# Performance work log

Measured on AMD Instinct MI355X. Metric: run time of the kernel, lower is better.

The kernel has to match this reference:

```python
import jax, jax.numpy as jnp
import numpy as np

ALPHA = 4.0  # spikingjelly surrogate.Sigmoid default
TAU = 2.0    # LIFNode default

@jax.custom_vjp
def spike(x):
    return (x >= 0).astype(x.dtype)

def _spike_fwd(x):
    return spike(x), x

def _spike_bwd(x, g):
    s = jax.nn.sigmoid(ALPHA * x)
    return (g * ALPHA * s * (1.0 - s),)

spike.defvjp(_spike_fwd, _spike_bwd)

def lif(x_seq, v_th):
    # multi-step LIF over leading time dim; decay_input=True, v_reset=0 (hard reset)
    def step(v, x):
        v = v + (x - v) / TAU
        s = spike(v - v_th)
        return v * (1.0 - s), s
    _, s_seq = jax.lax.scan(step, jnp.zeros_like(x_seq[0]), x_seq)
    return s_seq

def bn_c(x, gamma, beta, mean, var, eps=1e-5):
    # eval-mode BatchNorm1d over channel axis 2 of [T,N,C,V]
    inv = (gamma / jnp.sqrt(var + eps))[None, None, :, None]
    return (x - mean[None, None, :, None]) * inv + beta[None, None, :, None]

def conv1x1(x, w):
    # 1x1 Conv1d == channel mixing: w [Cout,Cin], x [T,N,C,V]
    return jnp.einsum('oc,tncv->tnov', w, x)

def setup_inputs() -> dict:
    key = jax.random.key(0)
    T, N, C, V = 4, 512, 256, 25
    ks = jax.random.split(key, 24)
    def bn_params(k1, k2, k3, k4):
        return (jax.random.uniform(k1, (C,)) * 0.5 + 0.75,
                jax.random.normal(k2, (C,)) * 0.1,
                jax.random.normal(k3, (C,)) * 0.1,
                jax.random.uniform(k4, (C,)) * 0.5 + 0.5)
    x = jax.random.normal(ks[0], (T, N, C, V), dtype=jnp.float32)
    s = 1.0 / np.sqrt(C)
    wq = jax.random.normal(ks[1], (C, C)) * s
    wk = jax.random.normal(ks[2], (C, C)) * s
    wv = jax.random.normal(ks[3], (C, C)) * s
    wp = jax.random.normal(ks[4], (C, C)) * s
    bp = jax.random.normal(ks[5], (C,)) * 0.02
    qg, qb, qm, qvar = bn_params(ks[6], ks[7], ks[8], ks[9])
    kg, kb, km, kvar = bn_params(ks[10], ks[11], ks[12], ks[13])
    vg, vb, vm, vvar = bn_params(ks[14], ks[15], ks[16], ks[17])
    pg, pb, pm, pvar = bn_params(ks[18], ks[19], ks[20], ks[21])
    return dict(x=x, wq=wq, wk=wk, wv=wv, wp=wp, bp=bp,
                qg=qg, qb=qb, qm=qm, qvar=qvar,
                kg=kg, kb=kb, km=km, kvar=kvar,
                vg=vg, vb=vb, vm=vm, vvar=vvar,
                pg=pg, pb=pb, pm=pm, pvar=pvar)

def reference(x, wq, wk, wv, wp, bp, qg, qb, qm, qvar, kg, kb, km, kvar,
              vg, vb, vm, vvar, pg, pb, pm, pvar):
    T, N, C, V = x.shape
    H = 8
    D = C // H
    scale = 0.125

    def branch(w, g, b, m, var):
        s = lif(bn_c(conv1x1(x, w), g, b, m, var), 1.0)       # [T,N,C,V]
        # -> [T,N,V,C] -> [T,N,V,H,D] -> [T,N,H,V,D]
        return jnp.transpose(s, (0, 1, 3, 2)).reshape(T, N, V, H, D).transpose(0, 1, 3, 2, 4)

    q = branch(wq, qg, qb, qm, qvar)
    k = branch(wk, kg, kb, km, kvar)
    v = branch(wv, vg, vb, vm, vvar)

    attn = jnp.einsum('tnhvd,tnhwd->tnhvw', q, k)            # binary spike attn, no softmax
    y = jnp.einsum('tnhvw,tnhwd->tnhvd', attn, v) * scale    # [T,N,H,V,D]
    y = y.transpose(0, 1, 2, 4, 3).reshape(T, N, C, V)       # transpose(3,4) then merge H*D=C
    y = lif(y, 0.5)                                          # attn_lif, v_threshold=0.5
    y = conv1x1(y, wp) + bp[None, None, :, None]             # proj_conv (bias=True)
    y = lif(bn_c(y, pg, pb, pm, pvar), 1.0)                  # proj_bn + proj_lif
    return y + x                                             # residual
```

## Files before the change

### kernel.cpp

```cpp
#include <hip/hip_runtime.h>
#include <cstdint>
#include <cstddef>

#define T_ 4
#define N_ 512
#define C_ 256
#define V_ 25
#define H_ 8

typedef _Float16 half8_t __attribute__((ext_vector_type(8)));
typedef float f32x16 __attribute__((ext_vector_type(16)));

__device__ __forceinline__ f32x16 mfma16(half8_t a, half8_t b, f32x16 c) {
  return __builtin_amdgcn_mfma_f32_32x32x16_f16(a, b, c, 0, 0, 0);
}

__global__ void kw_stage(const float* __restrict__ wq, const float* __restrict__ wk,
                         const float* __restrict__ wv, const float* __restrict__ wp,
                         const float* __restrict__ qg, const float* __restrict__ qvar,
                         const float* __restrict__ kg, const float* __restrict__ kvar,
                         const float* __restrict__ vg, const float* __restrict__ vvar,
                         const float* __restrict__ pg, const float* __restrict__ pvar,
                         _Float16* __restrict__ Wstg) {
  int i = blockIdx.x * 512 + threadIdx.x;
  int j = i & 7, lane = (i >> 3) & 63, rt = (i >> 9) & 3, m = (i >> 11) & 1;
  int s = (i >> 12) & 3, p = (i >> 14) & 3, c = i >> 16;
  int kt = p * 4 + s;
  int row = rt * 32 + (lane & 31);
  int k = kt * 16 + (lane >> 5) * 8 + j;
  const float *w, *g, *va;
  int grow;
  if (c < 6) {
    int br = c >> 1;
    w = br == 0 ? wq : br == 1 ? wk : wv;
    g = br == 0 ? qg : br == 1 ? kg : vg;
    va = br == 0 ? qvar : br == 1 ? kvar : vvar;
    grow = (c & 1) * 128 + row;
  } else {
    w = wp; g = pg; va = pvar;
    grow = (c - 6) * 128 + row;
  }
  float sc = g[grow] / sqrtf(va[grow] + 1e-5f);
  float wv_ = w[grow * 256 + k] * sc;
  _Float16 hi = (_Float16)wv_;
  Wstg[i] = (m == 0) ? hi : (_Float16)(wv_ - (float)hi);
}

#define STAGE_A(gidx, bufsel)                                                     \
  do {                                                                            \
    const _Float16* sp_ = Wstg + (size_t)(gidx) * 16384 + tid * 8;                \
    char* dp_ = Abuf + (bufsel) * 32768 + tid * 16;                               \
    __builtin_amdgcn_global_load_lds((const uint32_t*)(sp_),          (uint32_t*)(dp_),          16, 0, 0); \
    __builtin_amdgcn_global_load_lds((const uint32_t*)(sp_ + 4096),   (uint32_t*)(dp_ + 8192),   16, 0, 0); \
    __builtin_amdgcn_global_load_lds((const uint32_t*)(sp_ + 8192),   (uint32_t*)(dp_ + 16384),  16, 0, 0); \
    __builtin_amdgcn_global_load_lds((const uint32_t*)(sp_ + 12288),  (uint32_t*)(dp_ + 24576),  16, 0, 0); \
  } while (0)

__launch_bounds__(512, 1)
__global__ void k1_mfma(const float* __restrict__ x, const _Float16* __restrict__ Wstg,
                        const float* __restrict__ qg, const float* __restrict__ qb,
                        const float* __restrict__ qm, const float* __restrict__ qvar,
                        const float* __restrict__ kg, const float* __restrict__ kb,
                        const float* __restrict__ km, const float* __restrict__ kvar,
                        const float* __restrict__ vg, const float* __restrict__ vb,
                        const float* __restrict__ vm, const float* __restrict__ vvar,
                        uint32_t* __restrict__ masks) {
  __shared__ __align__(16) char LDSb[102400 + 25856 + 512];
  float* Xf = (float*)LDSb;
  char* Abuf = LDSb;
  float* Ms = (float*)(LDSb + 102400);
  float* bic = (float*)(LDSb + 102400 + 25856);

  const int n = blockIdx.x, tid = threadIdx.x;
  const int lane = tid & 63, wid = tid >> 6;
  const int rg = wid >> 2, cg = wid & 3;
  const int lr = lane & 31, lkg = lane >> 5;

  for (int t = 0; t < 4; ++t) {
    const float* sp = x + (size_t)(t * N_ + n) * 6400;
    float* dp = Xf + t * 6400;
    for (int i = tid; i < 1600; i += 512)
      __builtin_amdgcn_global_load_lds((const uint32_t*)(sp + i * 4), (uint32_t*)(dp + i * 4), 16, 0, 0);
  }
  __syncthreads();

  half8_t Bf0[16], Bf1[16];
  {
    int col = cg * 32 + lr;
    bool valid = col < 100;
    int tq = valid ? col / 25 : 0;
    int v = valid ? col - tq * 25 : 0;
    const float* xb = Xf + tq * 6400 + v;
#pragma unroll
    for (int kt = 0; kt < 16; ++kt) {
#pragma unroll
      for (int jj = 0; jj < 8; ++jj) {
        int k = kt * 16 + lkg * 8 + jj;
        float f = xb[k * 25];
        f = valid ? f : 0.0f;
        _Float16 hi = (_Float16)f;
        Bf0[kt][jj] = hi;
        Bf1[kt][jj] = (_Float16)(f - (float)hi);
      }
    }
  }
  __syncthreads();
  STAGE_A(0, 0);

  for (int c = 0; c < 6; ++c) {
    if (tid < 128) {
      int ch = (c & 1) * 128 + tid;
      const int br = c >> 1;
      const float* g  = br == 0 ? qg : br == 1 ? kg : vg;
      const float* be = br == 0 ? qb : br == 1 ? kb : vb;
      const float* mu = br == 0 ? qm : br == 1 ? km : vm;
      const float* va = br == 0 ? qvar : br == 1 ? kvar : vvar;
      float sc = g[ch] / sqrtf(va[ch] + 1e-5f);
      bic[tid] = be[ch] - mu[ch] * sc;
    }
    f32x16 acc0 = {}, acc1 = {};
#pragma unroll
    for (int p = 0; p < 4; ++p) {
      __syncthreads();
      int gnext = c * 4 + p + 1;
      if (gnext < 24) STAGE_A(gnext, (p + 1) & 1);
#pragma unroll
      for (int s = 0; s < 4; ++s) {
        const char* kb = Abuf + (p & 1) * 32768 + s * 8192;
        half8_t A00 = *(const half8_t*)(kb + 0    + 2 * rg * 1024 + lane * 16);
        half8_t A01 = *(const half8_t*)(kb + 0    + (2 * rg + 1) * 1024 + lane * 16);
        half8_t A10 = *(const half8_t*)(kb + 4096 + 2 * rg * 1024 + lane * 16);
        half8_t A11 = *(const half8_t*)(kb + 4096 + (2 * rg + 1) * 1024 + lane * 16);
        int kt = p * 4 + s;
        __builtin_amdgcn_s_setprio(1);
        acc0 = mfma16(A00, Bf0[kt], acc0);
        acc1 = mfma16(A01, Bf0[kt], acc1);
        acc0 = mfma16(A00, Bf1[kt], acc0);
        acc1 = mfma16(A01, Bf1[kt], acc1);
        acc0 = mfma16(A10, Bf0[kt], acc0);
        acc1 = mfma16(A11, Bf0[kt], acc1);
        __builtin_amdgcn_s_setprio(0);
      }
    }

    const int br = c >> 1;
    for (int ph = 0; ph < 2; ++ph) {
      __syncthreads();
      if (rg == ph) {
        int col = cg * 32 + lr;
        if (col < 100) {
#pragma unroll
          for (int rr = 0; rr < 16; ++rr) {
            int rowc = (rr & 3) + 8 * (rr >> 2) + 4 * lkg;
            Ms[rowc * 101 + col] = acc0[rr] + bic[ph * 64 + rowc];
            Ms[(32 + rowc) * 101 + col] = acc1[rr] + bic[ph * 64 + 32 + rowc];
          }
        }
      }
      __syncthreads();
      const int d = lane & 31, sub = lane >> 5;
      for (int it = 0; it < 4; ++it) {
        int ti = it * 16 + wid * 2 + sub;
        bool valid = ti < 50;
        int hl = valid ? ti / 25 : 0;
        int v = valid ? ti - hl * 25 : 0;
        int row = hl * 32 + d;
        float st = 0.0f;
#pragma unroll
        for (int t = 0; t < 4; ++t) {
          float cu = Ms[row * 101 + t * 25 + v];
          st += (cu - st) * 0.5f;
          bool sbit = valid && (st >= 1.0f);
          if (st >= 1.0f) st = 0.0f;
          unsigned long long b = __ballot(sbit);
          if (valid && (lane == 0 || lane == 32)) {
            uint32_t wd = (lane == 0) ? (uint32_t)b : (uint32_t)(b >> 32);
            int hg = (c & 1) * 4 + ph * 2 + hl;
            masks[((((size_t)t * N_ + n) * 3 + br) * H_ + hg) * V_ + v] = wd;
          }
        }
      }
    }
  }
}

__launch_bounds__(64)
__global__ void k2_attn(const uint32_t* __restrict__ masks, uint32_t* __restrict__ mask2) {
  __shared__ uint32_t qs[T_][V_], ks_[T_][V_], vs[T_][V_];
  const int n = blockIdx.x >> 3;
  const int h = blockIdx.x & 7;
  const int l = threadIdx.x;
  for (int i = l; i < T_ * 3 * V_; i += 64) {
    int t = i / (3 * V_);
    int r = i - t * (3 * V_);
    int br = r / V_;
    int v = r - br * V_;
    uint32_t w = masks[(((size_t)t * N_ + n) * 3 + br) * (H_ * V_) + h * V_ + v];
    if (br == 0) qs[t][v] = w;
    else if (br == 1) ks_[t][v] = w;
    else vs[t][v] = w;
  }
  __syncthreads();
  const int hi = l >> 5, d = l & 31;
  for (int vv = 0; vv < 13; ++vv) {
    int v = vv * 2 + hi;
    bool valid = (v < V_);
    int vc = valid ? v : 0;
    float st = 0.0f;
#pragma unroll
    for (int t = 0; t < 4; ++t) {
      int y = 0;
      uint32_t qmw = qs[t][vc];
#pragma unroll
      for (int w = 0; w < V_; ++w) {
        int a = __popc(qmw & ks_[t][w]);
        y += a * (int)((vs[t][w] >> d) & 1u);
      }
      float yf = 0.125f * (float)y;
      st += (yf - st) * 0.5f;
      bool s = valid && (st >= 0.5f);
      if (st >= 0.5f) st = 0.0f;
      unsigned long long b = __ballot(s);
      if (valid && (l == 0 || l == 32)) {
        uint32_t wd = (l == 0) ? (uint32_t)b : (uint32_t)(b >> 32);
        mask2[(((size_t)t * N_ + n) * V_ + v) * H_ + h] = wd;
      }
    }
  }
}

__launch_bounds__(512, 1)
__global__ void k3_mfma(const float* __restrict__ x, const _Float16* __restrict__ Wstg,
                        const uint32_t* __restrict__ mask2, const float* __restrict__ bp,
                        const float* __restrict__ pg, const float* __restrict__ pb,
                        const float* __restrict__ pm, const float* __restrict__ pvar,
                        float* __restrict__ out) {
  __shared__ __align__(16) char LDSb[65536 + 25856 + 512 + 3200];
  char* Abuf = LDSb;
  float* Ms = (float*)(LDSb + 65536);
  float* bic = (float*)(LDSb + 65536 + 25856);
  uint32_t* m2s = (uint32_t*)(LDSb + 65536 + 25856 + 512);

  const int n = blockIdx.x, tid = threadIdx.x;
  const int lane = tid & 63, wid = tid >> 6;
  const int rg = wid >> 2, cg = wid & 3;
  const int lr = lane & 31, lkg = lane >> 5;

  for (int i = tid; i < 800; i += 512) {
    int t = i / 200, r = i - t * 200;
    m2s[i] = mask2[(size_t)(t * N_ + n) * 200 + r];
  }
  __syncthreads();

  half8_t Bf[16];
  {
    int col = cg * 32 + lr;
    bool valid = col < 100;
    int tq = valid ? col / 25 : 0;
    int v = valid ? col - tq * 25 : 0;
#pragma unroll
    for (int kt = 0; kt < 16; ++kt) {
#pragma unroll
      for (int jj = 0; jj < 8; ++jj) {
        int k = kt * 16 + lkg * 8 + jj;
        uint32_t bit = (m2s[tq * 200 + v * 8 + (k >> 5)] >> (k & 31)) & 1u;
        Bf[kt][jj] = (valid && bit) ? (_Float16)1.0f : (_Float16)0.0f;
      }
    }
  }
  STAGE_A(24, 0);

  for (int c = 0; c < 2; ++c) {
    if (tid < 128) {
      int ch = c * 128 + tid;
      float sc = pg[ch] / sqrtf(pvar[ch] + 1e-5f);
      bic[tid] = fmaf(bp[ch] - pm[ch], sc, pb[ch]);
    }
    f32x16 acc0 = {}, acc1 = {};
#pragma unroll
    for (int p = 0; p < 4; ++p) {
      __syncthreads();
      int gnext = (6 + c) * 4 + p + 1;
      if (gnext < 32) STAGE_A(gnext, (p + 1) & 1);
#pragma unroll
      for (int s = 0; s < 4; ++s) {
        const char* kb = Abuf + (p & 1) * 32768 + s * 8192;
        half8_t A00 = *(const half8_t*)(kb + 0    + 2 * rg * 1024 + lane * 16);
        half8_t A01 = *(const half8_t*)(kb + 0    + (2 * rg + 1) * 1024 + lane * 16);
        half8_t A10 = *(const half8_t*)(kb + 4096 + 2 * rg * 1024 + lane * 16);
        half8_t A11 = *(const half8_t*)(kb + 4096 + (2 * rg + 1) * 1024 + lane * 16);
        int kt = p * 4 + s;
        __builtin_amdgcn_s_setprio(1);
        acc0 = mfma16(A00, Bf[kt], acc0);
        acc1 = mfma16(A01, Bf[kt], acc1);
        acc0 = mfma16(A10, Bf[kt], acc0);
        acc1 = mfma16(A11, Bf[kt], acc1);
        __builtin_amdgcn_s_setprio(0);
      }
    }

    for (int ph = 0; ph < 2; ++ph) {
      __syncthreads();
      if (rg == ph) {
        int col = cg * 32 + lr;
        if (col < 100) {
#pragma unroll
          for (int rr = 0; rr < 16; ++rr) {
            int rowc = (rr & 3) + 8 * (rr >> 2) + 4 * lkg;
            Ms[rowc * 101 + col] = acc0[rr] + bic[ph * 64 + rowc];
            Ms[(32 + rowc) * 101 + col] = acc1[rr] + bic[ph * 64 + 32 + rowc];
          }
        }
      }
      __syncthreads();
      const int d = lane & 31, sub = lane >> 5;
      for (int it = 0; it < 4; ++it) {
        int ti = it * 16 + wid * 2 + sub;
        if (ti < 50) {
          int hl = ti / 25, v = ti - hl * 25;
          int row = hl * 32 + d;
          float st = 0.0f;
#pragma unroll
          for (int t = 0; t < 4; ++t) {
            float cu = Ms[row * 101 + t * 25 + v];
            st += (cu - st) * 0.5f;
            float s = (st >= 1.0f) ? 1.0f : 0.0f;
            if (st >= 1.0f) st = 0.0f;
            Ms[row * 101 + t * 25 + v] = s;
          }
        }
      }
      __syncthreads();
      for (int ii = tid; ii < 6400; ii += 512) {
        int t = ii / 1600, r2 = ii - t * 1600;
        int cl = r2 / 25, v = r2 - cl * 25;
        size_t go = (size_t)(t * N_ + n) * 6400 + (size_t)(c * 128 + ph * 64 + cl) * 25 + v;
        out[go] = Ms[cl * 101 + t * 25 + v] + x[go];
      }
    }
  }
}

extern "C" void kernel_launch(void* const* d_in, const int* in_sizes, int n_in,
                              void* d_out, int out_size, void* d_ws, size_t ws_size,
                              hipStream_t stream) {
  const float* x    = (const float*)d_in[0];
  const float* wq   = (const float*)d_in[1];
  const float* wk   = (const float*)d_in[2];
  const float* wv   = (const float*)d_in[3];
  const float* wp   = (const float*)d_in[4];
  const float* bp   = (const float*)d_in[5];
  const float* qg   = (const float*)d_in[6];
  const float* qb   = (const float*)d_in[7];
  const float* qm   = (const float*)d_in[8];
  const float* qvar = (const float*)d_in[9];
  const float* kg   = (const float*)d_in[10];
  const float* kb   = (const float*)d_in[11];
  const float* km   = (const float*)d_in[12];
  const float* kvar = (const float*)d_in[13];
  const float* vg   = (const float*)d_in[14];
  const float* vb   = (const float*)d_in[15];
  const float* vm   = (const float*)d_in[16];
  const float* vvar = (const float*)d_in[17];
  const float* pg   = (const float*)d_in[18];
  const float* pb   = (const float*)d_in[19];
  const float* pm   = (const float*)d_in[20];
  const float* pvar = (const float*)d_in[21];

  _Float16* Wstg  = (_Float16*)d_ws;
  uint32_t* masks = (uint32_t*)d_ws + 262144;
  uint32_t* mask2 = masks + 1228800;

  kw_stage<<<1024, 512, 0, stream>>>(wq, wk, wv, wp, qg, qvar, kg, kvar,
                                     vg, vvar, pg, pvar, Wstg);
  k1_mfma<<<512, 512, 0, stream>>>(x, Wstg, qg, qb, qm, qvar, kg, kb, km, kvar,
                                   vg, vb, vm, vvar, masks);
  k2_attn<<<4096, 64, 0, stream>>>(masks, mask2);
  k3_mfma<<<512, 512, 0, stream>>>(x, Wstg, mask2, bp, pg, pb, pm, pvar, (float*)d_out);
}
```

Baseline: 275.0 us.

## Pre-split x into fp16 hi/lo staging and retile MFMA waves with swizzled LDS epilogue

Adds a kx_stage kernel that converts x to fp16 hi/lo pairs in a column-major (v,t)-ordered layout, so k1 loads its B fragments directly from global memory instead of staging fp32 x through LDS and splitting it in registers. Both k1 and k3 reassign waves so each wave owns one 32-row tile and two 32-column tiles, halving A-fragment LDS reads per MFMA. The full 128-row result is written to an XOR-swizzled LDS buffer with float4 stores in a single pass instead of two 64-row phases, and the BN bias is added in the LIF pass. The cost is an extra kernel launch and an extra global round trip for x (about 50MB of workspace), plus more B registers per thread.

```diff
diff --git a/kernel.cpp b/kernel.cpp
--- a/kernel.cpp
+++ b/kernel.cpp
@@ -46,6 +46,33 @@
   Wstg[i] = (m == 0) ? hi : (_Float16)(wv_ - (float)hi);
 }
 
+__global__ void kx_stage(const float* __restrict__ x, _Float16* __restrict__ X16) {
+  __shared__ float Xt[256 * 28];
+  const int n = blockIdx.x, tid = threadIdx.x;
+  for (int t = 0; t < 4; ++t) {
+    __syncthreads();
+    for (int i = tid; i < 6400; i += 256) {
+      int k = i / 25, v = i - k * 25;
+      Xt[k * 28 + v] = x[(size_t)(t * N_ + n) * 6400 + i];
+    }
+    __syncthreads();
+    for (int j = tid; j < 800; j += 256) {
+      int v = j >> 5, kb = j & 31, k0 = kb * 8;
+      half8_t hi, lo;
+#pragma unroll
+      for (int e = 0; e < 8; ++e) {
+        float f = Xt[(k0 + e) * 28 + v];
+        _Float16 h = (_Float16)f;
+        hi[e] = h;
+        lo[e] = (_Float16)(f - (float)h);
+      }
+      size_t base = ((size_t)(2 * n) * 100 + (v * 4 + t)) * 256 + k0;
+      *(half8_t*)(X16 + base) = hi;
+      *(half8_t*)(X16 + base + 25600) = lo;
+    }
+  }
+}
+
 #define STAGE_A(gidx, bufsel)                                                     \
   do {                                                                            \
     const _Float16* sp_ = Wstg + (size_t)(gidx) * 16384 + tid * 8;                \
@@ -56,8 +83,10 @@
     __builtin_amdgcn_global_load_lds((const uint32_t*)(sp_ + 12288),  (uint32_t*)(dp_ + 24576),  16, 0, 0); \
   } while (0)
 
+#define MS_BYTE(colx, rowx) ((colx) * 256 + (((rowx) * 4) ^ (((colx) & 7) << 4)))
+
 __launch_bounds__(512, 1)
-__global__ void k1_mfma(const float* __restrict__ x, const _Float16* __restrict__ Wstg,
+__global__ void k1_mfma(const _Float16* __restrict__ X16, const _Float16* __restrict__ Wstg,
                         const float* __restrict__ qg, const float* __restrict__ qb,
                         const float* __restrict__ qm, const float* __restrict__ qvar,
                         const float* __restrict__ kg, const float* __restrict__ kb,
@@ -65,119 +94,99 @@
                         const float* __restrict__ vg, const float* __restrict__ vb,
                         const float* __restrict__ vm, const float* __restrict__ vvar,
                         uint32_t* __restrict__ masks) {
-  __shared__ __align__(16) char LDSb[102400 + 25856 + 512];
-  float* Xf = (float*)LDSb;
+  __shared__ __align__(16) char LDSb[65536 + 32768 + 512];
   char* Abuf = LDSb;
-  float* Ms = (float*)(LDSb + 102400);
-  float* bic = (float*)(LDSb + 102400 + 25856);
+  char* MsB = LDSb + 65536;
+  float* bic = (float*)(LDSb + 65536 + 32768);
 
   const int n = blockIdx.x, tid = threadIdx.x;
   const int lane = tid & 63, wid = tid >> 6;
-  const int rg = wid >> 2, cg = wid & 3;
+  const int rt = wid & 3, cp = wid >> 2;
   const int lr = lane & 31, lkg = lane >> 5;
 
-  for (int t = 0; t < 4; ++t) {
-    const float* sp = x + (size_t)(t * N_ + n) * 6400;
-    float* dp = Xf + t * 6400;
-    for (int i = tid; i < 1600; i += 512)
-      __builtin_amdgcn_global_load_lds((const uint32_t*)(sp + i * 4), (uint32_t*)(dp + i * 4), 16, 0, 0);
-  }
-  __syncthreads();
-
-  half8_t Bf0[16], Bf1[16];
-  {
-    int col = cg * 32 + lr;
-    bool valid = col < 100;
-    int tq = valid ? col / 25 : 0;
-    int v = valid ? col - tq * 25 : 0;
-    const float* xb = Xf + tq * 6400 + v;
+  half8_t Bh[32], Bl[32];
+#pragma unroll
+  for (int ct = 0; ct < 2; ++ct) {
+    int col = cp * 64 + ct * 32 + lr;
+    int colc = col < 100 ? col : 99;
+    const _Float16* bp0 = X16 + ((size_t)(2 * n) * 100 + colc) * 256 + lkg * 8;
 #pragma unroll
     for (int kt = 0; kt < 16; ++kt) {
-#pragma unroll
-      for (int jj = 0; jj < 8; ++jj) {
-        int k = kt * 16 + lkg * 8 + jj;
-        float f = xb[k * 25];
-        f = valid ? f : 0.0f;
-        _Float16 hi = (_Float16)f;
-        Bf0[kt][jj] = hi;
-        Bf1[kt][jj] = (_Float16)(f - (float)hi);
-      }
-    }
-  }
-  __syncthreads();
+      Bh[ct * 16 + kt] = *(const half8_t*)(bp0 + kt * 16);
+      Bl[ct * 16 + kt] = *(const half8_t*)(bp0 + 25600 + kt * 16);
+    }
+  }
   STAGE_A(0, 0);
 
   for (int c = 0; c < 6; ++c) {
-    if (tid < 128) {
-      int ch = (c & 1) * 128 + tid;
-      const int br = c >> 1;
-      const float* g  = br == 0 ? qg : br == 1 ? kg : vg;
-      const float* be = br == 0 ? qb : br == 1 ? kb : vb;
-      const float* mu = br == 0 ? qm : br == 1 ? km : vm;
-      const float* va = br == 0 ? qvar : br == 1 ? kvar : vvar;
-      float sc = g[ch] / sqrtf(va[ch] + 1e-5f);
-      bic[tid] = be[ch] - mu[ch] * sc;
-    }
+    const int br = c >> 1;
     f32x16 acc0 = {}, acc1 = {};
 #pragma unroll
     for (int p = 0; p < 4; ++p) {
       __syncthreads();
+      if (p == 0 && tid < 128) {
+        int ch = (c & 1) * 128 + tid;
+        const float* g  = br == 0 ? qg : br == 1 ? kg : vg;
+        const float* be = br == 0 ? qb : br == 1 ? kb : vb;
+        const float* mu = br == 0 ? qm : br == 1 ? km : vm;
+        const float* va = br == 0 ? qvar : br == 1 ? kvar : vvar;
+        float sc = g[ch] / sqrtf(va[ch] + 1e-5f);
+        bic[tid] = be[ch] - mu[ch] * sc;
+      }
       int gnext = c * 4 + p + 1;
       if (gnext < 24) STAGE_A(gnext, (p + 1) & 1);
 #pragma unroll
       for (int s = 0; s < 4; ++s) {
-        const char* kb = Abuf + (p & 1) * 32768 + s * 8192;
-        half8_t A00 = *(const half8_t*)(kb + 0    + 2 * rg * 1024 + lane * 16);
-        half8_t A01 = *(const half8_t*)(kb + 0    + (2 * rg + 1) * 1024 + lane * 16);
-        half8_t A10 = *(const half8_t*)(kb + 4096 + 2 * rg * 1024 + lane * 16);
-        half8_t A11 = *(const half8_t*)(kb + 4096 + (2 * rg + 1) * 1024 + lane * 16);
-        int kt = p * 4 + s;
+        const char* kb = Abuf + (p & 1) * 32768 + s * 8192 + rt * 1024 + lane * 16;
+        half8_t Ahi = *(const half8_t*)(kb);
+        half8_t Alo = *(const half8_t*)(kb + 4096);
+        const int kt = p * 4 + s;
         __builtin_amdgcn_s_setprio(1);
-        acc0 = mfma16(A00, Bf0[kt], acc0);
-        acc1 = mfma16(A01, Bf0[kt], acc1);
-        acc0 = mfma16(A00, Bf1[kt], acc0);
-        acc1 = mfma16(A01, Bf1[kt], acc1);
-        acc0 = mfma16(A10, Bf0[kt], acc0);
-        acc1 = mfma16(A11, Bf0[kt], acc1);
+        acc0 = mfma16(Ahi, Bh[kt], acc0);
+        acc1 = mfma16(Ahi, Bh[16 + kt], acc1);
+        acc0 = mfma16(Ahi, Bl[kt], acc0);
+        acc1 = mfma16(Ahi, Bl[16 + kt], acc1);
+        acc0 = mfma16(Alo, Bh[kt], acc0);
+        acc1 = mfma16(Alo, Bh[16 + kt], acc1);
         __builtin_amdgcn_s_setprio(0);
       }
     }
 
-    const int br = c >> 1;
-    for (int ph = 0; ph < 2; ++ph) {
-      __syncthreads();
-      if (rg == ph) {
-        int col = cg * 32 + lr;
-        if (col < 100) {
-#pragma unroll
-          for (int rr = 0; rr < 16; ++rr) {
-            int rowc = (rr & 3) + 8 * (rr >> 2) + 4 * lkg;
-            Ms[rowc * 101 + col] = acc0[rr] + bic[ph * 64 + rowc];
-            Ms[(32 + rowc) * 101 + col] = acc1[rr] + bic[ph * 64 + 32 + rowc];
-          }
+    __syncthreads();
+#pragma unroll
+    for (int ct = 0; ct < 2; ++ct) {
+      int col = cp * 64 + ct * 32 + lr;
+      if (col < 100) {
+        f32x16 A = ct ? acc1 : acc0;
+#pragma unroll
+        for (int qq = 0; qq < 4; ++qq) {
+          int rowb = rt * 32 + qq * 8 + lkg * 4;
+          float4 vq = make_float4(A[qq * 4], A[qq * 4 + 1], A[qq * 4 + 2], A[qq * 4 + 3]);
+          *(float4*)(MsB + MS_BYTE(col, rowb)) = vq;
         }
       }
-      __syncthreads();
-      const int d = lane & 31, sub = lane >> 5;
-      for (int it = 0; it < 4; ++it) {
-        int ti = it * 16 + wid * 2 + sub;
-        bool valid = ti < 50;
-        int hl = valid ? ti / 25 : 0;
-        int v = valid ? ti - hl * 25 : 0;
-        int row = hl * 32 + d;
-        float st = 0.0f;
-#pragma unroll
-        for (int t = 0; t < 4; ++t) {
-          float cu = Ms[row * 101 + t * 25 + v];
-          st += (cu - st) * 0.5f;
-          bool sbit = valid && (st >= 1.0f);
-          if (st >= 1.0f) st = 0.0f;
-          unsigned long long b = __ballot(sbit);
-          if (valid && (lane == 0 || lane == 32)) {
-            uint32_t wd = (lane == 0) ? (uint32_t)b : (uint32_t)(b >> 32);
-            int hg = (c & 1) * 4 + ph * 2 + hl;
-            masks[((((size_t)t * N_ + n) * 3 + br) * H_ + hg) * V_ + v] = wd;
-          }
+    }
+    __syncthreads();
+    const int d = lane & 31, hl = lane >> 5;
+    for (int it = 0; it < 7; ++it) {
+      int task = it * 16 + wid * 2 + hl;
+      bool valid = task < 100;
+      int hg = valid ? task / 25 : 0;
+      int v = valid ? task - hg * 25 : 0;
+      int row = hg * 32 + d;
+      float bicv = bic[hg * 32 + d];
+      float st = 0.0f;
+#pragma unroll
+      for (int t = 0; t < 4; ++t) {
+        int colx = v * 4 + t;
+        float cu = *(const float*)(MsB + MS_BYTE(colx, row)) + bicv;
+        st += (cu - st) * 0.5f;
+        bool sb = valid && (st >= 1.0f);
+        if (st >= 1.0f) st = 0.0f;
+        unsigned long long b = __ballot(sb);
+        if (valid && (lane == 0 || lane == 32)) {
+          uint32_t wd = (lane == 0) ? (uint32_t)b : (uint32_t)(b >> 32);
+          masks[((((size_t)t * N_ + n) * 3 + br) * H_ + (c & 1) * 4 + hg) * V_ + v] = wd;
         }
       }
     }
@@ -235,15 +244,15 @@
                         const float* __restrict__ pg, const float* __restrict__ pb,
                         const float* __restrict__ pm, const float* __restrict__ pvar,
                         float* __restrict__ out) {
-  __shared__ __align__(16) char LDSb[65536 + 25856 + 512 + 3200];
+  __shared__ __align__(16) char LDSb[65536 + 32768 + 512 + 3200];
   char* Abuf = LDSb;
-  float* Ms = (float*)(LDSb + 65536);
-  float* bic = (float*)(LDSb + 65536 + 25856);
-  uint32_t* m2s = (uint32_t*)(LDSb + 65536 + 25856 + 512);
+  char* MsB = LDSb + 65536;
+  float* bic = (float*)(LDSb + 65536 + 32768);
+  uint32_t* m2s = (uint32_t*)(LDSb + 65536 + 32768 + 512);
 
   const int n = blockIdx.x, tid = threadIdx.x;
   const int lane = tid & 63, wid = tid >> 6;
-  const int rg = wid >> 2, cg = wid & 3;
+  const int rt = wid & 3, cp = wid >> 2;
   const int lr = lane & 31, lkg = lane >> 5;
 
   for (int i = tid; i < 800; i += 512) {
@@ -252,91 +261,97 @@
   }
   __syncthreads();
 
-  half8_t Bf[16];
-  {
-    int col = cg * 32 + lr;
+  half8_t Bb[32];
+#pragma unroll
+  for (int ct = 0; ct < 2; ++ct) {
+    int col = cp * 64 + ct * 32 + lr;
     bool valid = col < 100;
-    int tq = valid ? col / 25 : 0;
-    int v = valid ? col - tq * 25 : 0;
+    int v = valid ? (col >> 2) : 0;
+    int t = valid ? (col & 3) : 0;
 #pragma unroll
     for (int kt = 0; kt < 16; ++kt) {
 #pragma unroll
       for (int jj = 0; jj < 8; ++jj) {
         int k = kt * 16 + lkg * 8 + jj;
-        uint32_t bit = (m2s[tq * 200 + v * 8 + (k >> 5)] >> (k & 31)) & 1u;
-        Bf[kt][jj] = (valid && bit) ? (_Float16)1.0f : (_Float16)0.0f;
+        uint32_t bit = (m2s[t * 200 + v * 8 + (k >> 5)] >> (k & 31)) & 1u;
+        Bb[ct * 16 + kt][jj] = (valid && bit) ? (_Float16)1.0f : (_Float16)0.0f;
       }
     }
   }
   STAGE_A(24, 0);
 
   for (int c = 0; c < 2; ++c) {
-    if (tid < 128) {
-      int ch = c * 128 + tid;
-      float sc = pg[ch] / sqrtf(pvar[ch] + 1e-5f);
-      bic[tid] = fmaf(bp[ch] - pm[ch], sc, pb[ch]);
-    }
     f32x16 acc0 = {}, acc1 = {};
 #pragma unroll
     for (int p = 0; p < 4; ++p) {
       __syncthreads();
+      if (p == 0 && tid < 128) {
+        int ch = c * 128 + tid;
+        float sc = pg[ch] / sqrtf(pvar[ch] + 1e-5f);
+        bic[tid] = fmaf(bp[ch] - pm[ch], sc, pb[ch]);
+      }
       int gnext = (6 + c) * 4 + p + 1;
       if (gnext < 32) STAGE_A(gnext, (p + 1) & 1);
 #pragma unroll
       for (int s = 0; s < 4; ++s) {
-        const char* kb = Abuf + (p & 1) * 32768 + s * 8192;
-        half8_t A00 = *(const half8_t*)(kb + 0    + 2 * rg * 1024 + lane * 16);
-        half8_t A01 = *(const half8_t*)(kb + 0    + (2 * rg + 1) * 1024 + lane * 16);
-        half8_t A10 = *(const half8_t*)(kb + 4096 + 2 * rg * 1024 + lane * 16);
-        half8_t A11 = *(const half8_t*)(kb + 4096 + (2 * rg + 1) * 1024 + lane * 16);
-        int kt = p * 4 + s;
+        const char* kb = Abuf + (p & 1) * 32768 + s * 8192 + rt * 1024 + lane * 16;
+        half8_t Ahi = *(const half8_t*)(kb);
+        half8_t Alo = *(const half8_t*)(kb + 4096);
+        const int kt = p * 4 + s;
         __builtin_amdgcn_s_setprio(1);
-        acc0 = mfma16(A00, Bf[kt], acc0);
-        acc1 = mfma16(A01, Bf[kt], acc1);
-        acc0 = mfma16(A10, Bf[kt], acc0);
-        acc1 = mfma16(A11, Bf[kt], acc1);
+        acc0 = mfma16(Ahi, Bb[kt], acc0);
+        acc1 = mfma16(Ahi, Bb[16 + kt], acc1);
+        acc0 = mfma16(Alo, Bb[kt], acc0);
+        acc1 = mfma16(Alo, Bb[16 + kt], acc1);
         __builtin_amdgcn_s_setprio(0);
       }
     }
 
-    for (int ph = 0; ph < 2; ++ph) {
-      __syncthreads();
-      if (rg == ph) {
-        int col = cg * 32 + lr;
-        if (col < 100) {
-#pragma unroll
-          for (int rr = 0; rr < 16; ++rr) {
-            int rowc = (rr & 3) + 8 * (rr >> 2) + 4 * lkg;
-            Ms[rowc * 101 + col] = acc0[rr] + bic[ph * 64 + rowc];
-            Ms[(32 + rowc) * 101 + col] = acc1[rr] + bic[ph * 64 + 32 + rowc];
-          }
+    __syncthreads();
+#pragma unroll
+    for (int ct = 0; ct < 2; ++ct) {
+      int col = cp * 64 + ct * 32 + lr;
+      if (col < 100) {
+        f32x16 A = ct ? acc1 : acc0;
+#pragma unroll
+        for (int qq = 0; qq < 4; ++qq) {
+          int rowb = rt * 32 + qq * 8 + lkg * 4;
+          float4 vq = make_float4(A[qq * 4], A[qq * 4 + 1], A[qq * 4 + 2], A[qq * 4 + 3]);
+          *(float4*)(MsB + MS_BYTE(col, rowb)) = vq;
         }
       }
-      __syncthreads();
-      const int d = lane & 31, sub = lane >> 5;
-      for (int it = 0; it < 4; ++it) {
-        int ti = it * 16 + wid * 2 + sub;
-        if (ti < 50) {
-          int hl = ti / 25, v = ti - hl * 25;
-          int row = hl * 32 + d;
-          float st = 0.0f;
-#pragma unroll
-          for (int t = 0; t < 4; ++t) {
-            float cu = Ms[row * 101 + t * 25 + v];
-            st += (cu - st) * 0.5f;
-            float s = (st >= 1.0f) ? 1.0f : 0.0f;
-            if (st >= 1.0f) st = 0.0f;
-            Ms[row * 101 + t * 25 + v] = s;
-          }
+    }
+    __syncthreads();
+    const int d = lane & 31, hl = lane >> 5;
+    for (int it = 0; it < 7; ++it) {
+      int task = it * 16 + wid * 2 + hl;
+      bool valid = task < 100;
+      int hg = valid ? task / 25 : 0;
+      int v = valid ? task - hg * 25 : 0;
+      int row = hg * 32 + d;
+      float bicv = bic[hg * 32 + d];
+      float st = 0.0f;
+#pragma unroll
+      for (int t = 0; t < 4; ++t) {
+        int colx = v * 4 + t;
+        char* mp = MsB + MS_BYTE(colx, row);
+        if (valid) {
+          float cu = *(const float*)(mp) + bicv;
+          st += (cu - st) * 0.5f;
+          float sv = (st >= 1.0f) ? 1.0f : 0.0f;
+          if (st >= 1.0f) st = 0.0f;
+          *(float*)(mp) = sv;
         }
       }
-      __syncthreads();
-      for (int ii = tid; ii < 6400; ii += 512) {
-        int t = ii / 1600, r2 = ii - t * 1600;
-        int cl = r2 / 25, v = r2 - cl * 25;
-        size_t go = (size_t)(t * N_ + n) * 6400 + (size_t)(c * 128 + ph * 64 + cl) * 25 + v;
-        out[go] = Ms[cl * 101 + t * 25 + v] + x[go];
-      }
+    }
+    __syncthreads();
+    for (int ii = tid; ii < 12800; ii += 512) {
+      int t = ii / 3200, r2 = ii - t * 3200;
+      int cl = r2 / 25, v = r2 - cl * 25;
+      int colx = v * 4 + t;
+      float sv = *(const float*)(MsB + MS_BYTE(colx, cl));
+      size_t go = (size_t)(t * N_ + n) * 6400 + (size_t)(c * 128 + cl) * 25 + v;
+      out[go] = sv + x[go];
     }
   }
 }
@@ -367,13 +382,15 @@
   const float* pm   = (const float*)d_in[20];
   const float* pvar = (const float*)d_in[21];
 
-  _Float16* Wstg  = (_Float16*)d_ws;
-  uint32_t* masks = (uint32_t*)d_ws + 262144;
+  _Float16* Wstg = (_Float16*)d_ws;
+  _Float16* X16  = (_Float16*)d_ws + 524288;
+  uint32_t* masks = (uint32_t*)((char*)d_ws + 1048576 + 52428800);
   uint32_t* mask2 = masks + 1228800;
 
   kw_stage<<<1024, 512, 0, stream>>>(wq, wk, wv, wp, qg, qvar, kg, kvar,
                                      vg, vvar, pg, pvar, Wstg);
-  k1_mfma<<<512, 512, 0, stream>>>(x, Wstg, qg, qb, qm, qvar, kg, kb, km, kvar,
+  kx_stage<<<512, 256, 0, stream>>>(x, X16);
+  k1_mfma<<<512, 512, 0, stream>>>(X16, Wstg, qg, qb, qm, qvar, kg, kb, km, kvar,
                                    vg, vb, vm, vvar, masks);
   k2_attn<<<4096, 64, 0, stream>>>(masks, mask2);
   k3_mfma<<<512, 512, 0, stream>>>(x, Wstg, mask2, bp, pg, pb, pm, pvar, (float*)d_out);
```

New measurement: 458.9 us. 1.67x slower.
